# Kernel tuning notes

Measured on AMD Instinct MI355X. Metric: run time of the kernel, lower is better.

## Reference

```python
import jax, jax.numpy as jnp
import numpy as np

N_HEAD = 12


def build_mask(T, N):
    """Boolean mask, True = blocked. Mirrors st_mask construction for
    text_mask_mode='none', domain_present=None, text_to_motion_attn=False."""
    L = 3 * T + 5 * N
    r = jnp.arange(T)
    causal = r[:, None] >= r[None, :]          # allowed (lower-tri incl diag)
    strict = r[:, None] > r[None, :]           # allowed (strictly lower)
    m = jnp.zeros((L, L), dtype=bool)
    ml = 3 * T
    # motion-motion region starts fully blocked, then 7 sub-blocks opened
    m = m.at[:ml, :ml].set(True)
    m = m.at[0:T, 0:T].set(~causal)
    m = m.at[T:2 * T, 0:T].set(~causal)
    m = m.at[T:2 * T, T:2 * T].set(~strict)
    m = m.at[T:2 * T, 2 * T:3 * T].set(~strict)
    m = m.at[2 * T:3 * T, 0:T].set(~causal)
    m = m.at[2 * T:3 * T, T:2 * T].set(~causal)
    m = m.at[2 * T:3 * T, 2 * T:3 * T].set(~strict)
    # motion queries -> text keys: blocked by default
    m = m.at[:ml, ml:].set(True)
    # text queries -> motion keys: blocked (text_to_motion_attn=False)
    m = m.at[ml:, :ml].set(True)
    # text_mask_mode='none': up/down motion rows attend ALL text domains
    m = m.at[T:3 * T, ml:].set(False)
    return m


def setup_inputs() -> dict:
    key = jax.random.key(0)
    ks = jax.random.split(key, 9)
    C = 768
    B, T, N = 4, 512, 16
    L = 3 * T + 5 * N
    s = 1.0 / np.sqrt(C)
    return {
        "x": jax.random.normal(ks[0], (B, L, C), dtype=jnp.float32),
        "Wq": jax.random.normal(ks[1], (C, C), dtype=jnp.float32) * s,
        "bq": jax.random.normal(ks[2], (C,), dtype=jnp.float32) * 0.02,
        "Wk": jax.random.normal(ks[3], (C, C), dtype=jnp.float32) * s,
        "bk": jax.random.normal(ks[4], (C,), dtype=jnp.float32) * 0.02,
        "Wv": jax.random.normal(ks[5], (C, C), dtype=jnp.float32) * s,
        "bv": jax.random.normal(ks[6], (C,), dtype=jnp.float32) * 0.02,
        "Wp": jax.random.normal(ks[7], (C, C), dtype=jnp.float32) * s,
        "bp": jax.random.normal(ks[8], (C,), dtype=jnp.float32) * 0.02,
        "T_motion": 512,
        "N": 16,
    }


def reference(x, Wq, bq, Wk, bk, Wv, bv, Wp, bp, T_motion, N):
    B, L, C = x.shape
    nh = N_HEAD
    hd = C // nh
    # projections (torch Linear: x @ W.T + b)
    q = (x @ Wq.T + bq).reshape(B, L, nh, hd).transpose(0, 2, 1, 3)
    k = (x @ Wk.T + bk).reshape(B, L, nh, hd).transpose(0, 2, 1, 3)
    v = (x @ Wv.T + bv).reshape(B, L, nh, hd).transpose(0, 2, 1, 3)
    att = jnp.einsum('bhqd,bhkd->bhqk', q, k) * (1.0 / np.sqrt(hd))
    mask = build_mask(T_motion, N)                 # [L, L], True = blocked
    att = jnp.where(mask[None, None], -jnp.inf, att)
    att = jax.nn.softmax(att, axis=-1)
    y = jnp.einsum('bhqk,bhkd->bhqd', att, v)      # [B, nh, L, hd]
    y = y.transpose(0, 2, 1, 3).reshape(B, L, C)
    return y @ Wp.T + bp
```

## Files before the change

kernel.cpp:

```cpp
#include <hip/hip_runtime.h>

typedef _Float16 half8_t __attribute__((ext_vector_type(8)));
typedef _Float16 half4_t __attribute__((ext_vector_type(4)));
typedef int      int2_t  __attribute__((ext_vector_type(2)));
typedef float    f32x4   __attribute__((ext_vector_type(4)));

#define L_TOT 1616
#define ML    1536
#define TT    512
#define CDIM  768
#define HD    64
#define NH    12
#define MTOT  6464

#define QK_SCALE 0.1803368801f
#define FIXED_M 10.0f

__device__ __forceinline__ bool is_blocked(int i, int j) {
  if (j >= L_TOT) return true;
  if (i >= ML) return j < ML;
  if (j >= ML) return i < TT;
  int bi = i >> 9, bj = j >> 9;
  int a = i & 511, c = j & 511;
  if (bi == 0) return !(bj == 0 && c <= a);
  if (bi == 1) {
    if (bj == 0) return !(c <= a);
    return !(c < a);
  }
  if (bj == 2) return !(c < a);
  return !(c <= a);
}

__global__ __launch_bounds__(256) void cvt_kernel(
    const float* __restrict__ x, const float* __restrict__ wq,
    const float* __restrict__ wk, const float* __restrict__ wv,
    const float* __restrict__ wp, _Float16* __restrict__ Xh,
    _Float16* __restrict__ Wh)
{
  int a = blockIdx.y;
  const float* src; _Float16* dst; int n;
  if (a == 0) { src = x; dst = Xh; n = MTOT * CDIM; }
  else {
    src = (a == 1) ? wq : (a == 2) ? wk : (a == 3) ? wv : wp;
    dst = Wh + (size_t)(a - 1) * (CDIM * CDIM);
    n = CDIM * CDIM;
  }
  int i = (blockIdx.x * 256 + threadIdx.x) * 4;
  if (i < n) {
    float4 f = *(const float4*)(src + i);
    half4_t h;
    h[0] = (_Float16)f.x; h[1] = (_Float16)f.y;
    h[2] = (_Float16)f.z; h[3] = (_Float16)f.w;
    *(half4_t*)(dst + i) = h;
  }
}

__global__ __launch_bounds__(256) void gemm128_kernel(
    const _Float16* __restrict__ A, const _Float16* __restrict__ W,
    const float* __restrict__ bq, const float* __restrict__ bk,
    const float* __restrict__ bv, const float* __restrict__ bp,
    _Float16* __restrict__ Qh, _Float16* __restrict__ Kh,
    _Float16* __restrict__ Vt, float* __restrict__ Out, int fused)
{
  __shared__ __align__(16) _Float16 As[128 * 72];
  __shared__ __align__(16) _Float16 Bs[128 * 72];
  int tm = blockIdx.x, tn = blockIdx.y;
  int tid = threadIdx.x;
  int w = tid >> 6, lane = tid & 63;
  int wm = w & 1, wn = w >> 1;
  int lr = lane & 15, quad = lane >> 4;
  f32x4 acc[4][4];
#pragma unroll
  for (int i = 0; i < 4; i++)
#pragma unroll
    for (int j = 0; j < 4; j++) acc[i][j] = (f32x4){0.f, 0.f, 0.f, 0.f};
  int srow = tid >> 1, scol = (tid & 1) * 32;
  int arow = tm * 128 + srow; if (arow >= MTOT) arow = MTOT - 1;
  const _Float16* Ag = A + (size_t)arow * CDIM + scol;
  const _Float16* Bg = W + (size_t)(tn * 128 + srow) * CDIM + scol;
  _Float16* Asw = As + srow * 72 + scol;
  _Float16* Bsw = Bs + srow * 72 + scol;
  const _Float16* Arp = As + (wm * 64 + lr) * 72 + quad * 8;
  const _Float16* Brp = Bs + (wn * 64 + lr) * 72 + quad * 8;
  for (int k0 = 0; k0 < CDIM; k0 += 64) {
    __syncthreads();
#pragma unroll
    for (int u = 0; u < 4; u++) {
      *(int4*)(Asw + u * 8) = *(const int4*)(Ag + k0 + u * 8);
      *(int4*)(Bsw + u * 8) = *(const int4*)(Bg + k0 + u * 8);
    }
    __syncthreads();
#pragma unroll
    for (int kk = 0; kk < 64; kk += 32) {
      half8_t a[4], b[4];
#pragma unroll
      for (int g = 0; g < 4; g++) {
        a[g] = *(const half8_t*)(Arp + g * (16 * 72) + kk);
        b[g] = *(const half8_t*)(Brp + g * (16 * 72) + kk);
      }
#pragma unroll
      for (int mg = 0; mg < 4; mg++)
#pragma unroll
        for (int ng = 0; ng < 4; ng++)
          acc[mg][ng] = __builtin_amdgcn_mfma_f32_16x16x32_f16(a[mg], b[ng],
                                                               acc[mg][ng], 0, 0, 0);
    }
  }
  int mat, cbase;
  const float* bias;
  if (fused) { mat = tn / 6; cbase = (tn % 6) * 128;
               bias = (mat == 0) ? bq : (mat == 1) ? bk : bv; }
  else       { mat = 3; cbase = tn * 128; bias = bp; }
#pragma unroll
  for (int mg = 0; mg < 4; mg++) {
#pragma unroll
    for (int ng = 0; ng < 4; ng++) {
      int colt = wn * 64 + ng * 16 + lr;
      int c = cbase + colt;
      float bval = bias[c];
      int h = c >> 6, d = c & 63;
      int m0 = tm * 128 + wm * 64 + mg * 16 + quad * 4;
      if (mat == 3) {
        for (int r = 0; r < 4; r++) {
          int m = m0 + r;
          if (m < MTOT) Out[(size_t)m * CDIM + c] = acc[mg][ng][r] + bval;
        }
      } else if (mat == 2) {
        if (m0 < MTOT) {
          int b = m0 / L_TOT, l0 = m0 - b * L_TOT;
          half4_t hv;
          for (int r = 0; r < 4; r++) hv[r] = (_Float16)(acc[mg][ng][r] + bval);
          *(half4_t*)&Vt[((size_t)(b * NH + h) * HD + d) * L_TOT + l0] = hv;
        }
      } else {
        _Float16* dst = (mat == 0) ? Qh : Kh;
        for (int r = 0; r < 4; r++) {
          int m = m0 + r;
          if (m < MTOT) {
            int b = m / L_TOT, l = m - b * L_TOT;
            dst[((size_t)(b * NH + h) * L_TOT + l) * HD + d] = (_Float16)(acc[mg][ng][r] + bval);
          }
        }
      }
    }
  }
}

__global__ __launch_bounds__(256) void attn_kernel(
    const _Float16* __restrict__ Qh, const _Float16* __restrict__ Kh,
    const _Float16* __restrict__ Vt, _Float16* __restrict__ Yh)
{
  __shared__ __align__(16) _Float16 Ks[64 * 72];
  __shared__ __align__(16) _Float16 Vs[64 * 72];
  int qx = blockIdx.x;
  int qt = (qx < 24) ? (23 - qx) : qx;
  int bh = blockIdx.y;
  int b = bh / NH, h = bh - b * NH;
  const _Float16* Qb = Qh + (size_t)bh * L_TOT * HD;
  const _Float16* Kb = Kh + (size_t)bh * L_TOT * HD;
  const _Float16* Vb = Vt + (size_t)bh * HD * L_TOT;
  int tid = threadIdx.x;
  int w = tid >> 6, lane = tid & 63;
  int lr = lane & 15, quad = lane >> 4;

  int qrow = qt * 64 + w * 16 + lr;
  int qrc = qrow < L_TOT ? qrow : L_TOT - 1;
  half8_t qf0 = *(const half8_t*)(Qb + (size_t)qrc * HD + quad * 8);
  half8_t qf1 = *(const half8_t*)(Qb + (size_t)qrc * HD + 32 + quad * 8);
  {
    _Float16 sc = (_Float16)QK_SCALE;
#pragma unroll
    for (int j = 0; j < 8; j++) { qf0[j] *= sc; qf1[j] *= sc; }
  }

  float l_run = 0.f;
  f32x4 oacc[4];
  for (int mt = 0; mt < 4; mt++) oacc[mt] = (f32x4){0.f, 0.f, 0.f, 0.f};

  int srow = tid >> 2, scol8 = (tid & 3) * 8;
  int i_max = qt * 64 + 63; if (i_max >= L_TOT) i_max = L_TOT - 1;
  int i_min = qt * 64;

  for (int kt = 0; kt < 26; kt++) {
    int k0 = kt * 64;
    if (is_blocked(i_max, k0)) continue;
    bool full = (kt != 25) && !is_blocked(i_min, k0 + 63);
    __syncthreads();
    {
      int krow = k0 + srow; if (krow >= L_TOT) krow = L_TOT - 1;
      const _Float16* g = Kb + (size_t)krow * HD + scol8;
      _Float16* s = Ks + srow * 72 + scol8;
      *(int4*)s = *(const int4*)g;
      *(int4*)(s + 32) = *(const int4*)(g + 32);
      int vcol = k0 + scol8; if (vcol > L_TOT - 8) vcol = L_TOT - 8;
      const _Float16* gv = Vb + (size_t)srow * L_TOT + vcol;
      _Float16* sv = Vs + srow * 72 + scol8;
      *(int4*)sv = *(const int4*)gv;
      *(int4*)(sv + 32) = *(const int4*)(gv + 32);
    }
    __syncthreads();
    f32x4 s4[4];
#pragma unroll
    for (int cg = 0; cg < 4; cg++) {
      const _Float16* kp = Ks + (cg * 16 + lr) * 72 + quad * 8;
      half8_t kf0 = *(const half8_t*)kp;
      half8_t kf1 = *(const half8_t*)(kp + 32);
      f32x4 z = (f32x4){0.f, 0.f, 0.f, 0.f};
      z = __builtin_amdgcn_mfma_f32_16x16x32_f16(kf0, qf0, z, 0, 0, 0);
      z = __builtin_amdgcn_mfma_f32_16x16x32_f16(kf1, qf1, z, 0, 0, 0);
      s4[cg] = z;
    }
    if (!full) {
      int lo, hi;
      if (qrow >= L_TOT)      { lo = 0;  hi = -1; }
      else if (qrow >= ML)    { lo = ML; hi = L_TOT - 1; }
      else if (k0 >= ML)      { lo = 0;  hi = L_TOT - 1; }
      else {
        int bi = qrow >> 9, bj = k0 >> 9, a = qrow & 511;
        lo = 0;
        if (bi == 0 && bj > 0) hi = -1;
        else {
          int strict = (bj > 0 && !(bi == 2 && bj == 1)) ? 1 : 0;
          hi = bj * 512 + a - strict;
        }
      }
#pragma unroll
      for (int cg = 0; cg < 4; cg++) {
        int kb = k0 + cg * 16 + quad * 4;
#pragma unroll
        for (int r = 0; r < 4; r++) {
          int j = kb + r;
          if (j < lo || j > hi) s4[cg][r] = -1e30f;
        }
      }
    }
    int packed[8];
    float ladd = 0.f;
#pragma unroll
    for (int cg = 0; cg < 4; cg++) {
      float p0 = exp2f(s4[cg][0] - FIXED_M);
      float p1 = exp2f(s4[cg][1] - FIXED_M);
      float p2 = exp2f(s4[cg][2] - FIXED_M);
      float p3 = exp2f(s4[cg][3] - FIXED_M);
      ladd += (p0 + p1) + (p2 + p3);
      packed[cg * 2]     = __builtin_bit_cast(int, __builtin_amdgcn_cvt_pkrtz(p0, p1));
      packed[cg * 2 + 1] = __builtin_bit_cast(int, __builtin_amdgcn_cvt_pkrtz(p2, p3));
    }
    l_run += ladd;
#pragma unroll
    for (int cg = 0; cg < 4; cg++) {
      int2_t pi; pi[0] = packed[cg * 2]; pi[1] = packed[cg * 2 + 1];
      half4_t pb = __builtin_bit_cast(half4_t, pi);
      const _Float16* vbase = Vs + cg * 16 + quad * 4;
#pragma unroll
      for (int mt2 = 0; mt2 < 4; mt2++) {
        half4_t va = *(const half4_t*)(vbase + (mt2 * 16 + lr) * 72);
        oacc[mt2] = __builtin_amdgcn_mfma_f32_16x16x16f16(va, pb, oacc[mt2], 0, 0, 0);
      }
    }
  }
  l_run += __shfl_xor(l_run, 16);
  l_run += __shfl_xor(l_run, 32);
  __syncthreads();
  float inv = 1.f / l_run;
#pragma unroll
  for (int mt2 = 0; mt2 < 4; mt2++)
    for (int r = 0; r < 4; r++)
      Ks[(w * 16 + lr) * 72 + mt2 * 16 + quad * 4 + r] =
          (_Float16)(oacc[mt2][r] * inv);
  __syncthreads();
  {
    int rr = w * 16 + (lane >> 2);
    int cc = (lane & 3) * 16;
    int i = qt * 64 + rr;
    if (i < L_TOT) {
      const _Float16* srcp = Ks + rr * 72 + cc;
      int4 y0 = *(const int4*)srcp;
      int4 y1 = *(const int4*)(srcp + 8);
      _Float16* dst = Yh + ((size_t)(b * L_TOT) + i) * CDIM + h * HD + cc;
      *(int4*)dst = y0;
      *(int4*)(dst + 8) = y1;
    }
  }
}

extern "C" void kernel_launch(void* const* d_in, const int* in_sizes, int n_in,
                              void* d_out, int out_size, void* d_ws, size_t ws_size,
                              hipStream_t stream)
{
  const float* x  = (const float*)d_in[0];
  const float* Wq = (const float*)d_in[1];
  const float* bq = (const float*)d_in[2];
  const float* Wk = (const float*)d_in[3];
  const float* bk = (const float*)d_in[4];
  const float* Wv = (const float*)d_in[5];
  const float* bv = (const float*)d_in[6];
  const float* Wp = (const float*)d_in[7];
  const float* bp = (const float*)d_in[8];
  float* out = (float*)d_out;

  _Float16* ws = (_Float16*)d_ws;
  const size_t XN = (size_t)MTOT * CDIM;
  const size_t WN = (size_t)CDIM * CDIM;
  _Float16* Xh = ws;
  _Float16* Wh = Xh + XN;
  _Float16* Qh = Wh + 4 * WN;
  _Float16* Kh = Qh + XN;
  _Float16* Vt = Kh + XN;
  _Float16* Yh = Vt + XN;

  dim3 cvt_grid((unsigned)((XN / 4 + 255) / 256), 5);
  cvt_kernel<<<cvt_grid, 256, 0, stream>>>(x, Wq, Wk, Wv, Wp, Xh, Wh);
  gemm128_kernel<<<dim3(51, 18), 256, 0, stream>>>(Xh, Wh, bq, bk, bv, bp,
                                                   Qh, Kh, Vt, out, 1);
  attn_kernel<<<dim3(26, 48), 256, 0, stream>>>(Qh, Kh, Vt, Yh);
  gemm128_kernel<<<dim3(51, 6), 256, 0, stream>>>(Yh, Wh + 3 * WN, bq, bk, bv, bp,
                                                  Qh, Kh, Vt, out, 0);
}
```

Before: 241.8 us.

## Use direct global-to-LDS loads with XOR swizzle and 128-row attention query tiles

Replaces register-staged shared-memory fills in both the GEMM and attention kernels with global_load_lds 16-byte direct transfers into an XOR-swizzled unpadded LDS layout. The swizzle is meant to avoid bank conflicts without padding. The attention kernel now processes 128 query rows per block, two 16-row groups per wave, so each K/V tile loaded into LDS is reused twice as often. This halves the grid and raises register pressure, and it adds a separate output staging buffer.

```diff
diff --git a/kernel.cpp b/kernel.cpp
--- a/kernel.cpp
+++ b/kernel.cpp
@@ -15,6 +15,12 @@
 
 #define QK_SCALE 0.1803368801f
 #define FIXED_M 10.0f
+
+typedef __attribute__((address_space(3))) void  as3_void;
+typedef const __attribute__((address_space(1))) void as1_void;
+__device__ __forceinline__ void gload_lds16(const void* g, void* l) {
+  __builtin_amdgcn_global_load_lds((as1_void*)g, (as3_void*)l, 16, 0, 0);
+}
 
 __device__ __forceinline__ bool is_blocked(int i, int j) {
   if (j >= L_TOT) return true;
@@ -29,6 +35,21 @@
   }
   if (bj == 2) return !(c < a);
   return !(c <= a);
+}
+
+__device__ __forceinline__ void mask_interval(int qrow, int k0, int& lo, int& hi) {
+  lo = 0; hi = L_TOT - 1;
+  if (qrow >= L_TOT)      { hi = -1; }
+  else if (qrow >= ML)    { lo = ML; }
+  else if (k0 >= ML)      { }
+  else {
+    int bi = qrow >> 9, bj = k0 >> 9, a = qrow & 511;
+    if (bi == 0 && bj > 0) hi = -1;
+    else {
+      int strict = (bj > 0 && !(bi == 2 && bj == 1)) ? 1 : 0;
+      hi = bj * 512 + a - strict;
+    }
+  }
 }
 
 __global__ __launch_bounds__(256) void cvt_kernel(
@@ -62,8 +83,8 @@
     _Float16* __restrict__ Qh, _Float16* __restrict__ Kh,
     _Float16* __restrict__ Vt, float* __restrict__ Out, int fused)
 {
-  __shared__ __align__(16) _Float16 As[128 * 72];
-  __shared__ __align__(16) _Float16 Bs[128 * 72];
+  __shared__ __align__(16) _Float16 As[128 * 64];
+  __shared__ __align__(16) _Float16 Bs[128 * 64];
   int tm = blockIdx.x, tn = blockIdx.y;
   int tid = threadIdx.x;
   int w = tid >> 6, lane = tid & 63;
@@ -74,29 +95,31 @@
   for (int i = 0; i < 4; i++)
 #pragma unroll
     for (int j = 0; j < 4; j++) acc[i][j] = (f32x4){0.f, 0.f, 0.f, 0.f};
-  int srow = tid >> 1, scol = (tid & 1) * 32;
-  int arow = tm * 128 + srow; if (arow >= MTOT) arow = MTOT - 1;
-  const _Float16* Ag = A + (size_t)arow * CDIM + scol;
-  const _Float16* Bg = W + (size_t)(tn * 128 + srow) * CDIM + scol;
-  _Float16* Asw = As + srow * 72 + scol;
-  _Float16* Bsw = Bs + srow * 72 + scol;
-  const _Float16* Arp = As + (wm * 64 + lr) * 72 + quad * 8;
-  const _Float16* Brp = Bs + (wn * 64 + lr) * 72 + quad * 8;
+  int glog = ((lane & 7) ^ (lane >> 3)) * 8;
+  const _Float16* gA[4]; const _Float16* gB[4];
+#pragma unroll
+  for (int u = 0; u < 4; u++) {
+    int rl = (w * 4 + u) * 8 + (lane >> 3);
+    int ar = tm * 128 + rl; if (ar >= MTOT) ar = MTOT - 1;
+    gA[u] = A + (size_t)ar * CDIM + glog;
+    gB[u] = W + (size_t)(tn * 128 + rl) * CDIM + glog;
+  }
+  const int lsw = lr & 7;
   for (int k0 = 0; k0 < CDIM; k0 += 64) {
     __syncthreads();
 #pragma unroll
     for (int u = 0; u < 4; u++) {
-      *(int4*)(Asw + u * 8) = *(const int4*)(Ag + k0 + u * 8);
-      *(int4*)(Bsw + u * 8) = *(const int4*)(Bg + k0 + u * 8);
-    }
-    __syncthreads();
-#pragma unroll
-    for (int kk = 0; kk < 64; kk += 32) {
+      gload_lds16(gA[u] + k0, As + (w * 4 + u) * 512);
+      gload_lds16(gB[u] + k0, Bs + (w * 4 + u) * 512);
+    }
+    __syncthreads();
+#pragma unroll
+    for (int kg = 0; kg < 8; kg += 4) {
       half8_t a[4], b[4];
 #pragma unroll
       for (int g = 0; g < 4; g++) {
-        a[g] = *(const half8_t*)(Arp + g * (16 * 72) + kk);
-        b[g] = *(const half8_t*)(Brp + g * (16 * 72) + kk);
+        a[g] = *(const half8_t*)(As + (wm * 64 + g * 16 + lr) * 64 + (((quad + kg) ^ lsw) * 8));
+        b[g] = *(const half8_t*)(Bs + (wn * 64 + g * 16 + lr) * 64 + (((quad + kg) ^ lsw) * 8));
       }
 #pragma unroll
       for (int mg = 0; mg < 4; mg++)
@@ -150,10 +173,11 @@
     const _Float16* __restrict__ Qh, const _Float16* __restrict__ Kh,
     const _Float16* __restrict__ Vt, _Float16* __restrict__ Yh)
 {
-  __shared__ __align__(16) _Float16 Ks[64 * 72];
-  __shared__ __align__(16) _Float16 Vs[64 * 72];
+  __shared__ __align__(16) _Float16 Ks[64 * 64];
+  __shared__ __align__(16) _Float16 Vs[64 * 64];
+  __shared__ __align__(16) _Float16 Os[64 * 72];
   int qx = blockIdx.x;
-  int qt = (qx < 24) ? (23 - qx) : qx;
+  int qt = (qx < 12) ? (11 - qx) : 12;
   int bh = blockIdx.y;
   int b = bh / NH, h = bh - b * NH;
   const _Float16* Qb = Qh + (size_t)bh * L_TOT * HD;
@@ -162,119 +186,126 @@
   int tid = threadIdx.x;
   int w = tid >> 6, lane = tid & 63;
   int lr = lane & 15, quad = lane >> 4;
-
-  int qrow = qt * 64 + w * 16 + lr;
-  int qrc = qrow < L_TOT ? qrow : L_TOT - 1;
-  half8_t qf0 = *(const half8_t*)(Qb + (size_t)qrc * HD + quad * 8);
-  half8_t qf1 = *(const half8_t*)(Qb + (size_t)qrc * HD + 32 + quad * 8);
+  const int lsw = lr & 7;
+
+  int qrowA = qt * 128 + w * 32 + lr;
+  int qrowB = qrowA + 16;
+  int qrcA = qrowA < L_TOT ? qrowA : L_TOT - 1;
+  int qrcB = qrowB < L_TOT ? qrowB : L_TOT - 1;
+  half8_t qa0 = *(const half8_t*)(Qb + (size_t)qrcA * HD + quad * 8);
+  half8_t qa1 = *(const half8_t*)(Qb + (size_t)qrcA * HD + 32 + quad * 8);
+  half8_t qb0 = *(const half8_t*)(Qb + (size_t)qrcB * HD + quad * 8);
+  half8_t qb1 = *(const half8_t*)(Qb + (size_t)qrcB * HD + 32 + quad * 8);
   {
     _Float16 sc = (_Float16)QK_SCALE;
 #pragma unroll
-    for (int j = 0; j < 8; j++) { qf0[j] *= sc; qf1[j] *= sc; }
-  }
-
-  float l_run = 0.f;
-  f32x4 oacc[4];
-  for (int mt = 0; mt < 4; mt++) oacc[mt] = (f32x4){0.f, 0.f, 0.f, 0.f};
-
-  int srow = tid >> 2, scol8 = (tid & 3) * 8;
-  int i_max = qt * 64 + 63; if (i_max >= L_TOT) i_max = L_TOT - 1;
-  int i_min = qt * 64;
+    for (int j = 0; j < 8; j++) { qa0[j] *= sc; qa1[j] *= sc; qb0[j] *= sc; qb1[j] *= sc; }
+  }
+
+  float lA = 0.f, lB = 0.f;
+  f32x4 oA[4], oB[4];
+  for (int mt = 0; mt < 4; mt++) { oA[mt] = (f32x4){0.f,0.f,0.f,0.f}; oB[mt] = (f32x4){0.f,0.f,0.f,0.f}; }
+
+  int glog = ((lane & 7) ^ (lane >> 3)) * 8;
+  int srl[2];
+#pragma unroll
+  for (int u = 0; u < 2; u++) srl[u] = (w * 2 + u) * 8 + (lane >> 3);
+
+  int i_max = qt * 128 + 127; if (i_max >= L_TOT) i_max = L_TOT - 1;
+  int i_min = qt * 128;
 
   for (int kt = 0; kt < 26; kt++) {
     int k0 = kt * 64;
     if (is_blocked(i_max, k0)) continue;
     bool full = (kt != 25) && !is_blocked(i_min, k0 + 63);
     __syncthreads();
-    {
-      int krow = k0 + srow; if (krow >= L_TOT) krow = L_TOT - 1;
-      const _Float16* g = Kb + (size_t)krow * HD + scol8;
-      _Float16* s = Ks + srow * 72 + scol8;
-      *(int4*)s = *(const int4*)g;
-      *(int4*)(s + 32) = *(const int4*)(g + 32);
-      int vcol = k0 + scol8; if (vcol > L_TOT - 8) vcol = L_TOT - 8;
-      const _Float16* gv = Vb + (size_t)srow * L_TOT + vcol;
-      _Float16* sv = Vs + srow * 72 + scol8;
-      *(int4*)sv = *(const int4*)gv;
-      *(int4*)(sv + 32) = *(const int4*)(gv + 32);
-    }
-    __syncthreads();
-    f32x4 s4[4];
+#pragma unroll
+    for (int u = 0; u < 2; u++) {
+      int krow = k0 + srl[u]; if (krow >= L_TOT) krow = L_TOT - 1;
+      gload_lds16(Kb + (size_t)krow * HD + glog, Ks + (w * 2 + u) * 512);
+      int vc = k0 + glog; if (vc > L_TOT - 8) vc = L_TOT - 8;
+      gload_lds16(Vb + (size_t)srl[u] * L_TOT + vc, Vs + (w * 2 + u) * 512);
+    }
+    __syncthreads();
+    f32x4 sa[4], sb[4];
 #pragma unroll
     for (int cg = 0; cg < 4; cg++) {
-      const _Float16* kp = Ks + (cg * 16 + lr) * 72 + quad * 8;
-      half8_t kf0 = *(const half8_t*)kp;
-      half8_t kf1 = *(const half8_t*)(kp + 32);
-      f32x4 z = (f32x4){0.f, 0.f, 0.f, 0.f};
-      z = __builtin_amdgcn_mfma_f32_16x16x32_f16(kf0, qf0, z, 0, 0, 0);
-      z = __builtin_amdgcn_mfma_f32_16x16x32_f16(kf1, qf1, z, 0, 0, 0);
-      s4[cg] = z;
+      const _Float16* kp = Ks + (cg * 16 + lr) * 64;
+      half8_t kf0 = *(const half8_t*)(kp + ((quad ^ lsw) * 8));
+      half8_t kf1 = *(const half8_t*)(kp + (((quad + 4) ^ lsw) * 8));
+      f32x4 z = (f32x4){0.f,0.f,0.f,0.f};
+      z = __builtin_amdgcn_mfma_f32_16x16x32_f16(kf0, qa0, z, 0, 0, 0);
+      z = __builtin_amdgcn_mfma_f32_16x16x32_f16(kf1, qa1, z, 0, 0, 0);
+      sa[cg] = z;
+      z = (f32x4){0.f,0.f,0.f,0.f};
+      z = __builtin_amdgcn_mfma_f32_16x16x32_f16(kf0, qb0, z, 0, 0, 0);
+      z = __builtin_amdgcn_mfma_f32_16x16x32_f16(kf1, qb1, z, 0, 0, 0);
+      sb[cg] = z;
     }
     if (!full) {
-      int lo, hi;
-      if (qrow >= L_TOT)      { lo = 0;  hi = -1; }
-      else if (qrow >= ML)    { lo = ML; hi = L_TOT - 1; }
-      else if (k0 >= ML)      { lo = 0;  hi = L_TOT - 1; }
-      else {
-        int bi = qrow >> 9, bj = k0 >> 9, a = qrow & 511;
-        lo = 0;
-        if (bi == 0 && bj > 0) hi = -1;
-        else {
-          int strict = (bj > 0 && !(bi == 2 && bj == 1)) ? 1 : 0;
-          hi = bj * 512 + a - strict;
-        }
-      }
+      int loA, hiA, loB, hiB;
+      mask_interval(qrowA, k0, loA, hiA);
+      mask_interval(qrowB, k0, loB, hiB);
 #pragma unroll
       for (int cg = 0; cg < 4; cg++) {
         int kb = k0 + cg * 16 + quad * 4;
 #pragma unroll
         for (int r = 0; r < 4; r++) {
           int j = kb + r;
-          if (j < lo || j > hi) s4[cg][r] = -1e30f;
+          if (j < loA || j > hiA) sa[cg][r] = -1e30f;
+          if (j < loB || j > hiB) sb[cg][r] = -1e30f;
         }
       }
     }
-    int packed[8];
-    float ladd = 0.f;
+    int pkA[8], pkB[8];
 #pragma unroll
     for (int cg = 0; cg < 4; cg++) {
-      float p0 = exp2f(s4[cg][0] - FIXED_M);
-      float p1 = exp2f(s4[cg][1] - FIXED_M);
-      float p2 = exp2f(s4[cg][2] - FIXED_M);
-      float p3 = exp2f(s4[cg][3] - FIXED_M);
-      ladd += (p0 + p1) + (p2 + p3);
-      packed[cg * 2]     = __builtin_bit_cast(int, __builtin_amdgcn_cvt_pkrtz(p0, p1));
-      packed[cg * 2 + 1] = __builtin_bit_cast(int, __builtin_amdgcn_cvt_pkrtz(p2, p3));
-    }
-    l_run += ladd;
+      float a0 = exp2f(sa[cg][0] - FIXED_M), a1 = exp2f(sa[cg][1] - FIXED_M);
+      float a2 = exp2f(sa[cg][2] - FIXED_M), a3 = exp2f(sa[cg][3] - FIXED_M);
+      float b0 = exp2f(sb[cg][0] - FIXED_M), b1 = exp2f(sb[cg][1] - FIXED_M);
+      float b2 = exp2f(sb[cg][2] - FIXED_M), b3 = exp2f(sb[cg][3] - FIXED_M);
+      lA += (a0 + a1) + (a2 + a3);
+      lB += (b0 + b1) + (b2 + b3);
+      pkA[cg*2]   = __builtin_bit_cast(int, __builtin_amdgcn_cvt_pkrtz(a0, a1));
+      pkA[cg*2+1] = __builtin_bit_cast(int, __builtin_amdgcn_cvt_pkrtz(a2, a3));
+      pkB[cg*2]   = __builtin_bit_cast(int, __builtin_amdgcn_cvt_pkrtz(b0, b1));
+      pkB[cg*2+1] = __builtin_bit_cast(int, __builtin_amdgcn_cvt_pkrtz(b2, b3));
+    }
 #pragma unroll
     for (int cg = 0; cg < 4; cg++) {
-      int2_t pi; pi[0] = packed[cg * 2]; pi[1] = packed[cg * 2 + 1];
-      half4_t pb = __builtin_bit_cast(half4_t, pi);
-      const _Float16* vbase = Vs + cg * 16 + quad * 4;
+      int2_t pia; pia[0] = pkA[cg*2]; pia[1] = pkA[cg*2+1];
+      int2_t pib; pib[0] = pkB[cg*2]; pib[1] = pkB[cg*2+1];
+      half4_t pa = __builtin_bit_cast(half4_t, pia);
+      half4_t pb = __builtin_bit_cast(half4_t, pib);
+      int gph = ((2 * cg + (quad >> 1)) ^ lsw) * 8 + (quad & 1) * 4;
 #pragma unroll
       for (int mt2 = 0; mt2 < 4; mt2++) {
-        half4_t va = *(const half4_t*)(vbase + (mt2 * 16 + lr) * 72);
-        oacc[mt2] = __builtin_amdgcn_mfma_f32_16x16x16f16(va, pb, oacc[mt2], 0, 0, 0);
+        half4_t va = *(const half4_t*)(Vs + (mt2 * 16 + lr) * 64 + gph);
+        oA[mt2] = __builtin_amdgcn_mfma_f32_16x16x16f16(va, pa, oA[mt2], 0, 0, 0);
+        oB[mt2] = __builtin_amdgcn_mfma_f32_16x16x16f16(va, pb, oB[mt2], 0, 0, 0);
       }
     }
   }
-  l_run += __shfl_xor(l_run, 16);
-  l_run += __shfl_xor(l_run, 32);
-  __syncthreads();
-  float inv = 1.f / l_run;
-#pragma unroll
-  for (int mt2 = 0; mt2 < 4; mt2++)
-    for (int r = 0; r < 4; r++)
-      Ks[(w * 16 + lr) * 72 + mt2 * 16 + quad * 4 + r] =
-          (_Float16)(oacc[mt2][r] * inv);
-  __syncthreads();
-  {
+  lA += __shfl_xor(lA, 16); lA += __shfl_xor(lA, 32);
+  lB += __shfl_xor(lB, 16); lB += __shfl_xor(lB, 32);
+  float invA = 1.f / lA, invB = 1.f / lB;
+  for (int p = 0; p < 2; p++) {
+    __syncthreads();
+    if ((w >> 1) == p) {
+      int rb = (w & 1) * 32;
+#pragma unroll
+      for (int mt2 = 0; mt2 < 4; mt2++)
+        for (int r = 0; r < 4; r++) {
+          Os[(rb + lr) * 72 + mt2 * 16 + quad * 4 + r]      = (_Float16)(oA[mt2][r] * invA);
+          Os[(rb + 16 + lr) * 72 + mt2 * 16 + quad * 4 + r] = (_Float16)(oB[mt2][r] * invB);
+        }
+    }
+    __syncthreads();
     int rr = w * 16 + (lane >> 2);
     int cc = (lane & 3) * 16;
-    int i = qt * 64 + rr;
+    int i = qt * 128 + p * 64 + rr;
     if (i < L_TOT) {
-      const _Float16* srcp = Ks + rr * 72 + cc;
+      const _Float16* srcp = Os + rr * 72 + cc;
       int4 y0 = *(const int4*)srcp;
       int4 y1 = *(const int4*)(srcp + 8);
       _Float16* dst = Yh + ((size_t)(b * L_TOT) + i) * CDIM + h * HD + cc;
@@ -313,7 +344,7 @@
   cvt_kernel<<<cvt_grid, 256, 0, stream>>>(x, Wq, Wk, Wv, Wp, Xh, Wh);
   gemm128_kernel<<<dim3(51, 18), 256, 0, stream>>>(Xh, Wh, bq, bk, bv, bp,
                                                    Qh, Kh, Vt, out, 1);
-  attn_kernel<<<dim3(26, 48), 256, 0, stream>>>(Qh, Kh, Vt, Yh);
+  attn_kernel<<<dim3(13, 48), 256, 0, stream>>>(Qh, Kh, Vt, Yh);
   gemm128_kernel<<<dim3(51, 6), 256, 0, stream>>>(Yh, Wh + 3 * WN, bq, bk, bv, bp,
                                                   Qh, Kh, Vt, out, 0);
 }
```

Result: no change. 240.7 us (-0.4%).

## Use direct global-to-LDS loads with XOR-swizzled shared layout in GEMM and attention

Applied to the files above, without the earlier changes.

Replaces the register-staged global-to-shared copies in both the projection GEMM and the attention kernel with direct global_load_lds 16-byte transfers. The shared tiles drop their padding and use an XOR swizzle on 8-element groups so the MFMA fragment reads avoid bank conflicts. It also swaps exp2f for the hardware exp2 builtin and gives the attention output staging its own LDS buffer. This aims to cut VGPR use and instruction count in the load path. The trade-off is more complex per-lane address math and reliance on the direct-to-LDS load semantics lining up with the swizzled layout.

```diff
diff --git a/kernel.cpp b/kernel.cpp
--- a/kernel.cpp
+++ b/kernel.cpp
@@ -15,6 +15,18 @@
 
 #define QK_SCALE 0.1803368801f
 #define FIXED_M 10.0f
+
+#if __has_builtin(__builtin_amdgcn_exp2f)
+#define EXP2F(x) __builtin_amdgcn_exp2f(x)
+#else
+#define EXP2F(x) __expf((x) * 0.69314718056f)
+#endif
+
+typedef __attribute__((address_space(3))) void  as3_void;
+typedef const __attribute__((address_space(1))) void as1_void;
+__device__ __forceinline__ void gload_lds16(const void* g, void* l) {
+  __builtin_amdgcn_global_load_lds((as1_void*)g, (as3_void*)l, 16, 0, 0);
+}
 
 __device__ __forceinline__ bool is_blocked(int i, int j) {
   if (j >= L_TOT) return true;
@@ -29,6 +41,21 @@
   }
   if (bj == 2) return !(c < a);
   return !(c <= a);
+}
+
+__device__ __forceinline__ void mask_interval(int qrow, int k0, int& lo, int& hi) {
+  lo = 0; hi = L_TOT - 1;
+  if (qrow >= L_TOT)      { hi = -1; }
+  else if (qrow >= ML)    { lo = ML; }
+  else if (k0 >= ML)      { }
+  else {
+    int bi = qrow >> 9, bj = k0 >> 9, a = qrow & 511;
+    if (bi == 0 && bj > 0) hi = -1;
+    else {
+      int strict = (bj > 0 && !(bi == 2 && bj == 1)) ? 1 : 0;
+      hi = bj * 512 + a - strict;
+    }
+  }
 }
 
 __global__ __launch_bounds__(256) void cvt_kernel(
@@ -62,8 +89,8 @@
     _Float16* __restrict__ Qh, _Float16* __restrict__ Kh,
     _Float16* __restrict__ Vt, float* __restrict__ Out, int fused)
 {
-  __shared__ __align__(16) _Float16 As[128 * 72];
-  __shared__ __align__(16) _Float16 Bs[128 * 72];
+  __shared__ __align__(16) _Float16 As[128 * 64];
+  __shared__ __align__(16) _Float16 Bs[128 * 64];
   int tm = blockIdx.x, tn = blockIdx.y;
   int tid = threadIdx.x;
   int w = tid >> 6, lane = tid & 63;
@@ -74,29 +101,31 @@
   for (int i = 0; i < 4; i++)
 #pragma unroll
     for (int j = 0; j < 4; j++) acc[i][j] = (f32x4){0.f, 0.f, 0.f, 0.f};
-  int srow = tid >> 1, scol = (tid & 1) * 32;
-  int arow = tm * 128 + srow; if (arow >= MTOT) arow = MTOT - 1;
-  const _Float16* Ag = A + (size_t)arow * CDIM + scol;
-  const _Float16* Bg = W + (size_t)(tn * 128 + srow) * CDIM + scol;
-  _Float16* Asw = As + srow * 72 + scol;
-  _Float16* Bsw = Bs + srow * 72 + scol;
-  const _Float16* Arp = As + (wm * 64 + lr) * 72 + quad * 8;
-  const _Float16* Brp = Bs + (wn * 64 + lr) * 72 + quad * 8;
+  int glog = ((lane & 7) ^ (lane >> 3)) * 8;
+  const _Float16* gA[4]; const _Float16* gB[4];
+#pragma unroll
+  for (int u = 0; u < 4; u++) {
+    int rl = (w * 4 + u) * 8 + (lane >> 3);
+    int ar = tm * 128 + rl; if (ar >= MTOT) ar = MTOT - 1;
+    gA[u] = A + (size_t)ar * CDIM + glog;
+    gB[u] = W + (size_t)(tn * 128 + rl) * CDIM + glog;
+  }
+  const int lsw = lr & 7;
   for (int k0 = 0; k0 < CDIM; k0 += 64) {
     __syncthreads();
 #pragma unroll
     for (int u = 0; u < 4; u++) {
-      *(int4*)(Asw + u * 8) = *(const int4*)(Ag + k0 + u * 8);
-      *(int4*)(Bsw + u * 8) = *(const int4*)(Bg + k0 + u * 8);
+      gload_lds16(gA[u] + k0, As + (w * 4 + u) * 512);
+      gload_lds16(gB[u] + k0, Bs + (w * 4 + u) * 512);
     }
     __syncthreads();
 #pragma unroll
-    for (int kk = 0; kk < 64; kk += 32) {
+    for (int kg = 0; kg < 8; kg += 4) {
       half8_t a[4], b[4];
 #pragma unroll
       for (int g = 0; g < 4; g++) {
-        a[g] = *(const half8_t*)(Arp + g * (16 * 72) + kk);
-        b[g] = *(const half8_t*)(Brp + g * (16 * 72) + kk);
+        a[g] = *(const half8_t*)(As + (wm * 64 + g * 16 + lr) * 64 + (((quad + kg) ^ lsw) * 8));
+        b[g] = *(const half8_t*)(Bs + (wn * 64 + g * 16 + lr) * 64 + (((quad + kg) ^ lsw) * 8));
       }
 #pragma unroll
       for (int mg = 0; mg < 4; mg++)
@@ -150,8 +179,9 @@
     const _Float16* __restrict__ Qh, const _Float16* __restrict__ Kh,
     const _Float16* __restrict__ Vt, _Float16* __restrict__ Yh)
 {
-  __shared__ __align__(16) _Float16 Ks[64 * 72];
-  __shared__ __align__(16) _Float16 Vs[64 * 72];
+  __shared__ __align__(16) _Float16 Ks[64 * 64];
+  __shared__ __align__(16) _Float16 Vs[64 * 64];
+  __shared__ __align__(16) _Float16 Os[64 * 72];
   int qx = blockIdx.x;
   int qt = (qx < 24) ? (23 - qx) : qx;
   int bh = blockIdx.y;
@@ -162,6 +192,7 @@
   int tid = threadIdx.x;
   int w = tid >> 6, lane = tid & 63;
   int lr = lane & 15, quad = lane >> 4;
+  const int lsw = lr & 7;
 
   int qrow = qt * 64 + w * 16 + lr;
   int qrc = qrow < L_TOT ? qrow : L_TOT - 1;
@@ -177,7 +208,11 @@
   f32x4 oacc[4];
   for (int mt = 0; mt < 4; mt++) oacc[mt] = (f32x4){0.f, 0.f, 0.f, 0.f};
 
-  int srow = tid >> 2, scol8 = (tid & 3) * 8;
+  int glog = ((lane & 7) ^ (lane >> 3)) * 8;
+  int srl[2];
+#pragma unroll
+  for (int u = 0; u < 2; u++) srl[u] = (w * 2 + u) * 8 + (lane >> 3);
+
   int i_max = qt * 64 + 63; if (i_max >= L_TOT) i_max = L_TOT - 1;
   int i_min = qt * 64;
 
@@ -186,25 +221,20 @@
     if (is_blocked(i_max, k0)) continue;
     bool full = (kt != 25) && !is_blocked(i_min, k0 + 63);
     __syncthreads();
-    {
-      int krow = k0 + srow; if (krow >= L_TOT) krow = L_TOT - 1;
-      const _Float16* g = Kb + (size_t)krow * HD + scol8;
-      _Float16* s = Ks + srow * 72 + scol8;
-      *(int4*)s = *(const int4*)g;
-      *(int4*)(s + 32) = *(const int4*)(g + 32);
-      int vcol = k0 + scol8; if (vcol > L_TOT - 8) vcol = L_TOT - 8;
-      const _Float16* gv = Vb + (size_t)srow * L_TOT + vcol;
-      _Float16* sv = Vs + srow * 72 + scol8;
-      *(int4*)sv = *(const int4*)gv;
-      *(int4*)(sv + 32) = *(const int4*)(gv + 32);
+#pragma unroll
+    for (int u = 0; u < 2; u++) {
+      int krow = k0 + srl[u]; if (krow >= L_TOT) krow = L_TOT - 1;
+      gload_lds16(Kb + (size_t)krow * HD + glog, Ks + (w * 2 + u) * 512);
+      int vc = k0 + glog; if (vc > L_TOT - 8) vc = L_TOT - 8;
+      gload_lds16(Vb + (size_t)srl[u] * L_TOT + vc, Vs + (w * 2 + u) * 512);
     }
     __syncthreads();
     f32x4 s4[4];
 #pragma unroll
     for (int cg = 0; cg < 4; cg++) {
-      const _Float16* kp = Ks + (cg * 16 + lr) * 72 + quad * 8;
-      half8_t kf0 = *(const half8_t*)kp;
-      half8_t kf1 = *(const half8_t*)(kp + 32);
+      const _Float16* kp = Ks + (cg * 16 + lr) * 64;
+      half8_t kf0 = *(const half8_t*)(kp + ((quad ^ lsw) * 8));
+      half8_t kf1 = *(const half8_t*)(kp + (((quad + 4) ^ lsw) * 8));
       f32x4 z = (f32x4){0.f, 0.f, 0.f, 0.f};
       z = __builtin_amdgcn_mfma_f32_16x16x32_f16(kf0, qf0, z, 0, 0, 0);
       z = __builtin_amdgcn_mfma_f32_16x16x32_f16(kf1, qf1, z, 0, 0, 0);
@@ -212,18 +242,7 @@
     }
     if (!full) {
       int lo, hi;
-      if (qrow >= L_TOT)      { lo = 0;  hi = -1; }
-      else if (qrow >= ML)    { lo = ML; hi = L_TOT - 1; }
-      else if (k0 >= ML)      { lo = 0;  hi = L_TOT - 1; }
-      else {
-        int bi = qrow >> 9, bj = k0 >> 9, a = qrow & 511;
-        lo = 0;
-        if (bi == 0 && bj > 0) hi = -1;
-        else {
-          int strict = (bj > 0 && !(bi == 2 && bj == 1)) ? 1 : 0;
-          hi = bj * 512 + a - strict;
-        }
-      }
+      mask_interval(qrow, k0, lo, hi);
 #pragma unroll
       for (int cg = 0; cg < 4; cg++) {
         int kb = k0 + cg * 16 + quad * 4;
@@ -238,10 +257,10 @@
     float ladd = 0.f;
 #pragma unroll
     for (int cg = 0; cg < 4; cg++) {
-      float p0 = exp2f(s4[cg][0] - FIXED_M);
-      float p1 = exp2f(s4[cg][1] - FIXED_M);
-      float p2 = exp2f(s4[cg][2] - FIXED_M);
-      float p3 = exp2f(s4[cg][3] - FIXED_M);
+      float p0 = EXP2F(s4[cg][0] - FIXED_M);
+      float p1 = EXP2F(s4[cg][1] - FIXED_M);
+      float p2 = EXP2F(s4[cg][2] - FIXED_M);
+      float p3 = EXP2F(s4[cg][3] - FIXED_M);
       ladd += (p0 + p1) + (p2 + p3);
       packed[cg * 2]     = __builtin_bit_cast(int, __builtin_amdgcn_cvt_pkrtz(p0, p1));
       packed[cg * 2 + 1] = __builtin_bit_cast(int, __builtin_amdgcn_cvt_pkrtz(p2, p3));
@@ -251,10 +270,10 @@
     for (int cg = 0; cg < 4; cg++) {
       int2_t pi; pi[0] = packed[cg * 2]; pi[1] = packed[cg * 2 + 1];
       half4_t pb = __builtin_bit_cast(half4_t, pi);
-      const _Float16* vbase = Vs + cg * 16 + quad * 4;
+      int gph = ((2 * cg + (quad >> 1)) ^ lsw) * 8 + (quad & 1) * 4;
 #pragma unroll
       for (int mt2 = 0; mt2 < 4; mt2++) {
-        half4_t va = *(const half4_t*)(vbase + (mt2 * 16 + lr) * 72);
+        half4_t va = *(const half4_t*)(Vs + (mt2 * 16 + lr) * 64 + gph);
         oacc[mt2] = __builtin_amdgcn_mfma_f32_16x16x16f16(va, pb, oacc[mt2], 0, 0, 0);
       }
     }
@@ -266,7 +285,7 @@
 #pragma unroll
   for (int mt2 = 0; mt2 < 4; mt2++)
     for (int r = 0; r < 4; r++)
-      Ks[(w * 16 + lr) * 72 + mt2 * 16 + quad * 4 + r] =
+      Os[(w * 16 + lr) * 72 + mt2 * 16 + quad * 4 + r] =
           (_Float16)(oacc[mt2][r] * inv);
   __syncthreads();
   {
@@ -274,7 +293,7 @@
     int cc = (lane & 3) * 16;
     int i = qt * 64 + rr;
     if (i < L_TOT) {
-      const _Float16* srcp = Ks + rr * 72 + cc;
+      const _Float16* srcp = Os + rr * 72 + cc;
       int4 y0 = *(const int4*)srcp;
       int4 y1 = *(const int4*)(srcp + 8);
       _Float16* dst = Yh + ((size_t)(b * L_TOT) + i) * CDIM + h * HD + cc;
```

After: 218.1 us. 1.11x faster.
